# Performance work log

Hardware: AMD Instinct MI355X
Metric: run time of the kernel (lower is better)

Reference implementation:

```python
import jax, jax.numpy as jnp
import numpy as np

B, C, H, W = 8, 256, 128, 128
BN_EPS = 1e-5

def setup_inputs() -> dict:
    key = jax.random.key(0)
    ks = jax.random.split(key, 7)
    scale = 1.0 / np.sqrt(C)
    x = jax.random.normal(ks[0], (B, C, H, W), dtype=jnp.float32)
    w_qkv = jax.random.normal(ks[1], (3 * C, C), dtype=jnp.float32) * scale
    w_proj = jax.random.normal(ks[2], (C, C), dtype=jnp.float32) * scale
    gamma = jax.random.uniform(ks[3], (C,), dtype=jnp.float32)
    beta = jax.random.normal(ks[4], (C,), dtype=jnp.float32)
    running_mean = jax.random.normal(ks[5], (C,), dtype=jnp.float32)
    running_var = jax.random.uniform(ks[6], (C,), dtype=jnp.float32) + 0.5
    return {"x": x, "w_qkv": w_qkv, "w_proj": w_proj, "gamma": gamma,
            "beta": beta, "running_mean": running_mean, "running_var": running_var}

def reference(x, w_qkv, w_proj, gamma, beta, running_mean, running_var):
    b, c, h, w = x.shape
    n = h * w
    xf = x.reshape(b, c, n)                       # flatten spatial
    # 1x1 conv == channel matmul: [3c,c] x [b,c,n] -> [b,3c,n]
    qkv = jnp.einsum('oc,bcn->bon', w_qkv, xf)
    q, k, v = jnp.split(qkv, 3, axis=1)           # each [b,c,n]
    k = jax.nn.softmax(k, axis=-1)                # softmax over spatial
    context = jnp.einsum('bcn,bdn->bcd', k, v)    # k @ v^T, [b,c,c]
    out = jnp.einsum('bcd,bcn->bdn', context, q)  # context^T @ q, [b,c,n]
    out = jnp.einsum('oc,bcn->bon', w_proj, out)  # 1x1 proj
    # BatchNorm (inference form with running stats)
    inv = gamma / jnp.sqrt(running_var + BN_EPS)
    out = out * inv[None, :, None] + (beta - running_mean * inv)[None, :, None]
    out = jax.nn.relu(out)
    return out.reshape(b, c, h, w)
```

## Files before the change

### kernel.cpp

```cpp
#include <hip/hip_runtime.h>
#include <stdint.h>

#define B_   8
#define C_   256
#define N_   16384

typedef __attribute__((ext_vector_type(8))) short bf16x8;
typedef __attribute__((ext_vector_type(4))) float f32x4;

__device__ inline float bf2f(unsigned short h) {
    return __uint_as_float(((unsigned)h) << 16);
}
__device__ inline unsigned short f2bf(float f) {
    unsigned u = __float_as_uint(f);
    u += 0x7FFF + ((u >> 16) & 1);
    return (unsigned short)(u >> 16);
}

__device__ inline void gl_lds16(const void* g, void* l) {
    __builtin_amdgcn_global_load_lds(
        reinterpret_cast<const __attribute__((address_space(1))) unsigned int*>(
            reinterpret_cast<uintptr_t>(g)),
        reinterpret_cast<__attribute__((address_space(3))) unsigned int*>(
            reinterpret_cast<uintptr_t>(l)),
        16, 0, 0);
}

__device__ inline f32x4 mfma16(bf16x8 a, bf16x8 b, f32x4 c) {
    return __builtin_amdgcn_mfma_f32_16x16x32_bf16(a, b, c, 0, 0, 0);
}

__global__ __launch_bounds__(256) void k1_transpose(const float* __restrict__ x,
                                                    unsigned short* __restrict__ xT) {
    __shared__ unsigned short tile[64][65];
    const int b = blockIdx.z, c0 = blockIdx.y * 64, n0 = blockIdx.x * 64;
    const float* xb = x + (size_t)b * C_ * N_;
    const int t = threadIdx.x;
    const int tr = t >> 4, tc4 = (t & 15) * 4;
#pragma unroll
    for (int p = 0; p < 4; p++) {
        const int i = p * 16 + tr;
        const float4 v = *(const float4*)(xb + (size_t)(c0 + i) * N_ + n0 + tc4);
        tile[i][tc4 + 0] = f2bf(v.x);
        tile[i][tc4 + 1] = f2bf(v.y);
        tile[i][tc4 + 2] = f2bf(v.z);
        tile[i][tc4 + 3] = f2bf(v.w);
    }
    __syncthreads();
    unsigned short* xTb = xT + (size_t)b * N_ * C_;
#pragma unroll
    for (int p = 0; p < 4; p++) {
        const int jj = p * 16 + tr;
        ushort4 o;
        o.x = tile[tc4 + 0][jj];
        o.y = tile[tc4 + 1][jj];
        o.z = tile[tc4 + 2][jj];
        o.w = tile[tc4 + 3][jj];
        *(ushort4*)(xTb + (size_t)(n0 + jj) * C_ + c0 + tc4) = o;
    }
}

__global__ __launch_bounds__(256) void k1b_setup(const float* __restrict__ wqkv,
                                                 const float* __restrict__ gamma,
                                                 const float* __restrict__ beta,
                                                 const float* __restrict__ rmean,
                                                 const float* __restrict__ rvar,
                                                 unsigned short* __restrict__ wqkv_bf,
                                                 float* __restrict__ inv,
                                                 float* __restrict__ b2) {
    const int t = threadIdx.x;
    if (blockIdx.x < 192) {
        const int base = blockIdx.x * 1024 + t * 4;
        const float4 v = *(const float4*)(wqkv + base);
        ushort4 o;
        o.x = f2bf(v.x); o.y = f2bf(v.y); o.z = f2bf(v.z); o.w = f2bf(v.w);
        *(ushort4*)(wqkv_bf + base) = o;
    } else {
        const float iv = gamma[t] * rsqrtf(rvar[t] + 1e-5f);
        inv[t] = iv;
        b2[t]  = beta[t] - rmean[t] * iv;
    }
}

__global__ __launch_bounds__(256) void k2_kv(const unsigned short* __restrict__ Wkv,
                                             const unsigned short* __restrict__ xT,
                                             unsigned short* __restrict__ kL,
                                             unsigned short* __restrict__ v) {
    __shared__ __align__(16) unsigned short As[128 * 32];
    __shared__ __align__(16) unsigned short Bs[128 * 32];
    const int b  = blockIdx.z;
    const int m0 = blockIdx.y * 128;
    const int n0 = blockIdx.x * 128;
    const int t = threadIdx.x, wave = t >> 6, lane = t & 63;
    const int wm = wave >> 1, wn = wave & 1;

    const unsigned short* xTb = xT + (size_t)b * N_ * C_;

    const int ch1 = wave * 64 + lane, ch2 = ch1 + 256;
    const int r1 = ch1 >> 2, q1 = ch1 & 3;
    const int r2 = ch2 >> 2, q2 = ch2 & 3;
    unsigned short* ldsA1 = As + wave * 512;
    unsigned short* ldsA2 = As + 2048 + wave * 512;
    unsigned short* ldsB1 = Bs + wave * 512;
    unsigned short* ldsB2 = Bs + 2048 + wave * 512;

    f32x4 acc[4][4];
#pragma unroll
    for (int i = 0; i < 4; i++)
#pragma unroll
        for (int j = 0; j < 4; j++)
#pragma unroll
            for (int r = 0; r < 4; r++) acc[i][j][r] = 0.f;

    const int fr = lane & 15;
    const int fk = (lane >> 4) * 8;

    for (int kk = 0; kk < 256; kk += 32) {
        __syncthreads();
        gl_lds16(Wkv + (size_t)(m0 + r1) * 256 + kk + q1 * 8, ldsA1);
        gl_lds16(Wkv + (size_t)(m0 + r2) * 256 + kk + q2 * 8, ldsA2);
        gl_lds16(xTb + (size_t)(n0 + r1) * 256 + kk + q1 * 8, ldsB1);
        gl_lds16(xTb + (size_t)(n0 + r2) * 256 + kk + q2 * 8, ldsB2);
        __syncthreads();
        bf16x8 af[4], bfv[4];
#pragma unroll
        for (int i = 0; i < 4; i++)
            af[i] = *(const bf16x8*)(As + (wm * 64 + i * 16 + fr) * 32 + fk);
#pragma unroll
        for (int j = 0; j < 4; j++)
            bfv[j] = *(const bf16x8*)(Bs + (wn * 64 + j * 16 + fr) * 32 + fk);
#pragma unroll
        for (int i = 0; i < 4; i++)
#pragma unroll
            for (int j = 0; j < 4; j++)
                acc[i][j] = mfma16(af[i], bfv[j], acc[i][j]);
    }

    const int col = lane & 15, rowq = (lane >> 4) * 4;
    unsigned short* outK = kL + (size_t)b * C_ * N_;
    unsigned short* outV = v  + (size_t)b * C_ * N_;
#pragma unroll
    for (int i = 0; i < 4; i++) {
        const int gm = m0 + wm * 64 + i * 16 + rowq;
#pragma unroll
        for (int j = 0; j < 4; j++) {
            const int gn = n0 + wn * 64 + j * 16 + col;
#pragma unroll
            for (int r = 0; r < 4; r++) {
                const int m = gm + r;
                const unsigned short hv = f2bf(acc[i][j][r]);
                if (m < 256) outK[(size_t)m * N_ + gn] = hv;
                else         outV[(size_t)(m - 256) * N_ + gn] = hv;
            }
        }
    }
}

__global__ __launch_bounds__(256) void k3_stats(const unsigned short* __restrict__ kL,
                                                float* __restrict__ rmax,
                                                float* __restrict__ rsum) {
    const size_t rowbase = (size_t)blockIdx.x * N_;
    const int t = threadIdx.x;
    uint4 d[8];
#pragma unroll
    for (int i = 0; i < 8; i++)
        d[i] = *(const uint4*)(kL + rowbase + (size_t)(i * 256 + t) * 8);
    float m = -3.4e38f;
#pragma unroll
    for (int i = 0; i < 8; i++) {
        const unsigned short* p = (const unsigned short*)&d[i];
#pragma unroll
        for (int e = 0; e < 8; e++) m = fmaxf(m, bf2f(p[e]));
    }
#pragma unroll
    for (int o = 1; o < 64; o <<= 1) m = fmaxf(m, __shfl_xor(m, o, 64));
    __shared__ float red[4];
    __shared__ float red2[4];
    if ((t & 63) == 0) red[t >> 6] = m;
    __syncthreads();
    m = fmaxf(fmaxf(red[0], red[1]), fmaxf(red[2], red[3]));
    float s = 0.f;
#pragma unroll
    for (int i = 0; i < 8; i++) {
        const unsigned short* p = (const unsigned short*)&d[i];
#pragma unroll
        for (int e = 0; e < 8; e++) s += __expf(bf2f(p[e]) - m);
    }
#pragma unroll
    for (int o = 1; o < 64; o <<= 1) s += __shfl_xor(s, o, 64);
    if ((t & 63) == 0) red2[t >> 6] = s;
    __syncthreads();
    if (t == 0) {
        rmax[blockIdx.x] = m;
        rsum[blockIdx.x] = red2[0] + red2[1] + red2[2] + red2[3];
    }
}

__global__ __launch_bounds__(256) void k4_ctx(const unsigned short* __restrict__ kL,
                                              const unsigned short* __restrict__ v,
                                              const float* __restrict__ rmax,
                                              float* __restrict__ ctx) {
    __shared__ __align__(16) unsigned short As[128 * 32];
    __shared__ __align__(16) unsigned short Bs[128 * 32];
    const int bz = blockIdx.z;
    const int b = bz >> 3, s = bz & 7;
    const int m0 = blockIdx.y * 128;
    const int n0 = blockIdx.x * 128;
    const int t = threadIdx.x, wave = t >> 6, lane = t & 63;
    const int wm = wave >> 1, wn = wave & 1;

    const unsigned short* kb = kL + (size_t)b * C_ * N_;
    const unsigned short* vb = v  + (size_t)b * C_ * N_;

    const int ch1 = wave * 64 + lane, ch2 = ch1 + 256;
    const int r1 = ch1 >> 2, q1 = ch1 & 3;
    const int r2 = ch2 >> 2, q2 = ch2 & 3;
    const float mx1 = rmax[b * 256 + m0 + r1];
    const float mx2 = rmax[b * 256 + m0 + r2];
    unsigned short* ldsB1 = Bs + wave * 512;
    unsigned short* ldsB2 = Bs + 2048 + wave * 512;

    f32x4 acc[4][4];
#pragma unroll
    for (int i = 0; i < 4; i++)
#pragma unroll
        for (int j = 0; j < 4; j++)
#pragma unroll
            for (int r = 0; r < 4; r++) acc[i][j][r] = 0.f;

    const int fr = lane & 15;
    const int fk = (lane >> 4) * 8;
    const int kbase = s * 2048;

    for (int kk = kbase; kk < kbase + 2048; kk += 32) {
        __syncthreads();
        gl_lds16(vb + (size_t)(n0 + r1) * N_ + kk + q1 * 8, ldsB1);
        gl_lds16(vb + (size_t)(n0 + r2) * N_ + kk + q2 * 8, ldsB2);
        const uint4 a1 = *(const uint4*)(kb + (size_t)(m0 + r1) * N_ + kk + q1 * 8);
        const uint4 a2 = *(const uint4*)(kb + (size_t)(m0 + r2) * N_ + kk + q2 * 8);
        uint4 e1, e2;
        {
            const unsigned short* p = (const unsigned short*)&a1;
            unsigned short* o = (unsigned short*)&e1;
#pragma unroll
            for (int e = 0; e < 8; e++) o[e] = f2bf(__expf(bf2f(p[e]) - mx1));
        }
        {
            const unsigned short* p = (const unsigned short*)&a2;
            unsigned short* o = (unsigned short*)&e2;
#pragma unroll
            for (int e = 0; e < 8; e++) o[e] = f2bf(__expf(bf2f(p[e]) - mx2));
        }
        *(uint4*)(As + r1 * 32 + q1 * 8) = e1;
        *(uint4*)(As + r2 * 32 + q2 * 8) = e2;
        __syncthreads();
        bf16x8 af[4], bfv[4];
#pragma unroll
        for (int i = 0; i < 4; i++)
            af[i] = *(const bf16x8*)(As + (wm * 64 + i * 16 + fr) * 32 + fk);
#pragma unroll
        for (int j = 0; j < 4; j++)
            bfv[j] = *(const bf16x8*)(Bs + (wn * 64 + j * 16 + fr) * 32 + fk);
#pragma unroll
        for (int i = 0; i < 4; i++)
#pragma unroll
            for (int j = 0; j < 4; j++)
                acc[i][j] = mfma16(af[i], bfv[j], acc[i][j]);
    }

    float* cb = ctx + (size_t)b * C_ * C_;
    const int col = lane & 15, rowq = (lane >> 4) * 4;
#pragma unroll
    for (int i = 0; i < 4; i++) {
        const int gc = m0 + wm * 64 + i * 16 + rowq;
#pragma unroll
        for (int j = 0; j < 4; j++) {
            const int gd = n0 + wn * 64 + j * 16 + col;
#pragma unroll
            for (int r = 0; r < 4; r++)
                atomicAdd(&cb[(size_t)(gc + r) * C_ + gd], acc[i][j][r]);
        }
    }
}

__global__ __launch_bounds__(256) void k5a_T(const float* __restrict__ Wp,
                                             const float* __restrict__ ctx,
                                             const float* __restrict__ rsum,
                                             float* __restrict__ T) {
    __shared__ float Asm[64][65];
    __shared__ float Bsm[64][65];
    const int b = blockIdx.z;
    const int o0 = blockIdx.y * 64, c0 = blockIdx.x * 64;
    const int t = threadIdx.x;
    const int tm = t >> 4, tn = t & 15;
    const int lc4 = tn * 4;
    float acc[4][4] = {};
    const float* cb = ctx + (size_t)b * C_ * C_;
    for (int kk = 0; kk < 256; kk += 64) {
        __syncthreads();
#pragma unroll
        for (int p = 0; p < 4; p++) {
            const int r = p * 16 + tm;
            const float4 av = *(const float4*)(Wp + (size_t)(o0 + r) * C_ + kk + lc4);
            Asm[r][lc4] = av.x; Asm[r][lc4 + 1] = av.y; Asm[r][lc4 + 2] = av.z; Asm[r][lc4 + 3] = av.w;
            const float4 bv = *(const float4*)(cb + (size_t)(c0 + r) * C_ + kk + lc4);
            Bsm[r][lc4] = bv.x; Bsm[r][lc4 + 1] = bv.y; Bsm[r][lc4 + 2] = bv.z; Bsm[r][lc4 + 3] = bv.w;
        }
        __syncthreads();
        for (int k = 0; k < 64; k++) {
            float a_[4], b_[4];
#pragma unroll
            for (int i = 0; i < 4; i++) a_[i] = Asm[tm * 4 + i][k];
#pragma unroll
            for (int j = 0; j < 4; j++) b_[j] = Bsm[tn * 4 + j][k];
#pragma unroll
            for (int i = 0; i < 4; i++)
#pragma unroll
                for (int j = 0; j < 4; j++) acc[i][j] += a_[i] * b_[j];
        }
    }
    float isv[4];
#pragma unroll
    for (int j = 0; j < 4; j++) isv[j] = 1.f / rsum[b * 256 + c0 + tn * 4 + j];
#pragma unroll
    for (int i = 0; i < 4; i++)
#pragma unroll
        for (int j = 0; j < 4; j++)
            T[((size_t)b * C_ + o0 + tm * 4 + i) * C_ + c0 + tn * 4 + j] = acc[i][j] * isv[j];
}

__global__ __launch_bounds__(256) void k5b_G(const float* __restrict__ Tm,
                                             const float* __restrict__ Wq,
                                             const float* __restrict__ inv,
                                             unsigned short* __restrict__ G) {
    __shared__ float Asm[64][65];
    __shared__ float Bsm[64][65];
    const int b = blockIdx.z;
    const int o0 = blockIdx.y * 64, j0 = blockIdx.x * 64;
    const int t = threadIdx.x;
    const int tm = t >> 4, tn = t & 15;
    const int lc4 = tn * 4;
    float acc[4][4] = {};
    const float* Tb = Tm + (size_t)b * C_ * C_;
    for (int kk = 0; kk < 256; kk += 64) {
        __syncthreads();
#pragma unroll
        for (int p = 0; p < 4; p++) {
            const int r = p * 16 + tm;
            const float4 av = *(const float4*)(Tb + (size_t)(o0 + r) * C_ + kk + lc4);
            Asm[r][lc4] = av.x; Asm[r][lc4 + 1] = av.y; Asm[r][lc4 + 2] = av.z; Asm[r][lc4 + 3] = av.w;
            const float4 bv = *(const float4*)(Wq + (size_t)(kk + r) * C_ + j0 + lc4);
            Bsm[r][lc4] = bv.x; Bsm[r][lc4 + 1] = bv.y; Bsm[r][lc4 + 2] = bv.z; Bsm[r][lc4 + 3] = bv.w;
        }
        __syncthreads();
        for (int k = 0; k < 64; k++) {
            float a_[4], b_[4];
#pragma unroll
            for (int i = 0; i < 4; i++) a_[i] = Asm[tm * 4 + i][k];
#pragma unroll
            for (int j = 0; j < 4; j++) b_[j] = Bsm[k][tn * 4 + j];
#pragma unroll
            for (int i = 0; i < 4; i++)
#pragma unroll
                for (int j = 0; j < 4; j++) acc[i][j] += a_[i] * b_[j];
        }
    }
#pragma unroll
    for (int i = 0; i < 4; i++) {
        const float iv = inv[o0 + tm * 4 + i];
#pragma unroll
        for (int j = 0; j < 4; j++)
            G[((size_t)b * C_ + o0 + tm * 4 + i) * C_ + j0 + tn * 4 + j] = f2bf(acc[i][j] * iv);
    }
}

__global__ __launch_bounds__(256) void k6_out(const unsigned short* __restrict__ G,
                                              const unsigned short* __restrict__ xT,
                                              const float* __restrict__ b2,
                                              float* __restrict__ out) {
    __shared__ __align__(16) unsigned short As[128 * 32];
    __shared__ __align__(16) unsigned short Bs[128 * 32];
    const int b  = blockIdx.z;
    const int m0 = blockIdx.y * 128;
    const int n0 = blockIdx.x * 128;
    const int t = threadIdx.x, wave = t >> 6, lane = t & 63;
    const int wm = wave >> 1, wn = wave & 1;

    const unsigned short* Gb  = G  + (size_t)b * C_ * C_;
    const unsigned short* xTb = xT + (size_t)b * N_ * C_;

    const int ch1 = wave * 64 + lane, ch2 = ch1 + 256;
    const int r1 = ch1 >> 2, q1 = ch1 & 3;
    const int r2 = ch2 >> 2, q2 = ch2 & 3;
    unsigned short* ldsA1 = As + wave * 512;
    unsigned short* ldsA2 = As + 2048 + wave * 512;
    unsigned short* ldsB1 = Bs + wave * 512;
    unsigned short* ldsB2 = Bs + 2048 + wave * 512;

    f32x4 acc[4][4];
#pragma unroll
    for (int i = 0; i < 4; i++)
#pragma unroll
        for (int j = 0; j < 4; j++)
#pragma unroll
            for (int r = 0; r < 4; r++) acc[i][j][r] = 0.f;

    const int fr = lane & 15;
    const int fk = (lane >> 4) * 8;

    for (int kk = 0; kk < 256; kk += 32) {
        __syncthreads();
        gl_lds16(Gb  + (size_t)(m0 + r1) * 256 + kk + q1 * 8, ldsA1);
        gl_lds16(Gb  + (size_t)(m0 + r2) * 256 + kk + q2 * 8, ldsA2);
        gl_lds16(xTb + (size_t)(n0 + r1) * 256 + kk + q1 * 8, ldsB1);
        gl_lds16(xTb + (size_t)(n0 + r2) * 256 + kk + q2 * 8, ldsB2);
        __syncthreads();
        bf16x8 af[4], bfv[4];
#pragma unroll
        for (int i = 0; i < 4; i++)
            af[i] = *(const bf16x8*)(As + (wm * 64 + i * 16 + fr) * 32 + fk);
#pragma unroll
        for (int j = 0; j < 4; j++)
            bfv[j] = *(const bf16x8*)(Bs + (wn * 64 + j * 16 + fr) * 32 + fk);
#pragma unroll
        for (int i = 0; i < 4; i++)
#pragma unroll
            for (int j = 0; j < 4; j++)
                acc[i][j] = mfma16(af[i], bfv[j], acc[i][j]);
    }

    const int col = lane & 15, rowq = (lane >> 4) * 4;
    float* ob = out + (size_t)b * C_ * N_;
#pragma unroll
    for (int i = 0; i < 4; i++) {
        const int gm = m0 + wm * 64 + i * 16 + rowq;
#pragma unroll
        for (int j = 0; j < 4; j++) {
            const int gn = n0 + wn * 64 + j * 16 + col;
#pragma unroll
            for (int r = 0; r < 4; r++) {
                const float val = fmaxf(acc[i][j][r] + b2[gm + r], 0.f);
                ob[(size_t)(gm + r) * N_ + gn] = val;
            }
        }
    }
}

extern "C" void kernel_launch(void* const* d_in, const int* in_sizes, int n_in,
                              void* d_out, int out_size, void* d_ws, size_t ws_size,
                              hipStream_t stream) {
    const float* x     = (const float*)d_in[0];
    const float* wqkv  = (const float*)d_in[1];
    const float* wproj = (const float*)d_in[2];
    const float* gamma = (const float*)d_in[3];
    const float* beta  = (const float*)d_in[4];
    const float* rmean = (const float*)d_in[5];
    const float* rvar  = (const float*)d_in[6];
    float* out = (float*)d_out;

    char* ws = (char*)d_ws;
    size_t off = 0;
    auto alloc = [&](size_t bytes) {
        void* p = ws + off;
        off += (bytes + 255) & ~(size_t)255;
        return p;
    };
    unsigned short* xT      = (unsigned short*)alloc((size_t)B_ * N_ * C_ * 2);
    unsigned short* kL      = (unsigned short*)alloc((size_t)B_ * C_ * N_ * 2);
    unsigned short* vv      = (unsigned short*)alloc((size_t)B_ * C_ * N_ * 2);
    unsigned short* wqkv_bf = (unsigned short*)alloc((size_t)768 * 256 * 2);
    float* rmax = (float*)alloc(2048 * 4);
    float* rsum = (float*)alloc(2048 * 4);
    float* invp = (float*)alloc(256 * 4);
    float* b2p  = (float*)alloc(256 * 4);
    float* ctx  = (float*)alloc((size_t)B_ * C_ * C_ * 4);
    float* Tm   = (float*)alloc((size_t)B_ * C_ * C_ * 4);
    unsigned short* G = (unsigned short*)alloc((size_t)B_ * C_ * C_ * 2);

    hipLaunchKernelGGL(k1_transpose, dim3(256, 4, 8), dim3(256), 0, stream, x, xT);
    hipLaunchKernelGGL(k1b_setup, dim3(193), dim3(256), 0, stream,
                       wqkv, gamma, beta, rmean, rvar, wqkv_bf, invp, b2p);
    hipLaunchKernelGGL(k2_kv, dim3(128, 4, 8), dim3(256), 0, stream,
                       wqkv_bf + 256 * 256, xT, kL, vv);
    hipLaunchKernelGGL(k3_stats, dim3(2048), dim3(256), 0, stream, kL, rmax, rsum);
    hipMemsetAsync(ctx, 0, (size_t)B_ * C_ * C_ * 4, stream);
    hipLaunchKernelGGL(k4_ctx, dim3(2, 2, 64), dim3(256), 0, stream, kL, vv, rmax, ctx);
    hipLaunchKernelGGL(k5a_T, dim3(4, 4, 8), dim3(256), 0, stream, wproj, ctx, rsum, Tm);
    hipLaunchKernelGGL(k5b_G, dim3(4, 4, 8), dim3(256), 0, stream, Tm, wqkv, invp, G);
    hipLaunchKernelGGL(k6_out, dim3(128, 2, 8), dim3(256), 0, stream, G, xT, b2p, out);
}
```

Measured before the change: 447.7 us.

## Fuse softmax stats into KV GEMM and context kernels, stage full xT tile

Removes the separate k3_stats pass. The row max is now computed in the k2 epilogue through an order-preserving uint atomicMax, and the exp-sum is accumulated inside k4_ctx with atomicAdd. k2 and k6 now load a whole 128x256 bf16 xT tile into LDS once and loop over all output-channel chunks, reading the weight operands straight from global memory. This removes one full read of K and the repeated xT loads, at the cost of 64KB of LDS per block (lower occupancy), uncached global weight fragment loads, and atomics on the row statistics.

```diff
diff --git a/kernel.cpp b/kernel.cpp
--- a/kernel.cpp
+++ b/kernel.cpp
@@ -15,6 +15,14 @@
     unsigned u = __float_as_uint(f);
     u += 0x7FFF + ((u >> 16) & 1);
     return (unsigned short)(u >> 16);
+}
+__device__ inline unsigned fkey(float f) {
+    unsigned u = __float_as_uint(f);
+    return (u & 0x80000000u) ? ~u : (u | 0x80000000u);
+}
+__device__ inline float funkey(unsigned k) {
+    unsigned u = (k & 0x80000000u) ? (k ^ 0x80000000u) : ~k;
+    return __uint_as_float(u);
 }
 
 __device__ inline void gl_lds16(const void* g, void* l) {
@@ -85,121 +93,96 @@
 __global__ __launch_bounds__(256) void k2_kv(const unsigned short* __restrict__ Wkv,
                                              const unsigned short* __restrict__ xT,
                                              unsigned short* __restrict__ kL,
-                                             unsigned short* __restrict__ v) {
-    __shared__ __align__(16) unsigned short As[128 * 32];
-    __shared__ __align__(16) unsigned short Bs[128 * 32];
-    const int b  = blockIdx.z;
-    const int m0 = blockIdx.y * 128;
+                                             unsigned short* __restrict__ vv,
+                                             unsigned int* __restrict__ rmaxU) {
+    __shared__ __align__(16) unsigned short Bs[128 * 256];
+    const int b  = blockIdx.y;
     const int n0 = blockIdx.x * 128;
     const int t = threadIdx.x, wave = t >> 6, lane = t & 63;
     const int wm = wave >> 1, wn = wave & 1;
 
-    const unsigned short* xTb = xT + (size_t)b * N_ * C_;
-
-    const int ch1 = wave * 64 + lane, ch2 = ch1 + 256;
-    const int r1 = ch1 >> 2, q1 = ch1 & 3;
-    const int r2 = ch2 >> 2, q2 = ch2 & 3;
-    unsigned short* ldsA1 = As + wave * 512;
-    unsigned short* ldsA2 = As + 2048 + wave * 512;
-    unsigned short* ldsB1 = Bs + wave * 512;
-    unsigned short* ldsB2 = Bs + 2048 + wave * 512;
-
-    f32x4 acc[4][4];
-#pragma unroll
-    for (int i = 0; i < 4; i++)
-#pragma unroll
-        for (int j = 0; j < 4; j++)
-#pragma unroll
-            for (int r = 0; r < 4; r++) acc[i][j][r] = 0.f;
+    const unsigned short* xTb = xT + (size_t)b * N_ * C_ + (size_t)n0 * C_;
+#pragma unroll
+    for (int rnd = 0; rnd < 16; rnd++) {
+        gl_lds16(xTb + rnd * 2048 + wave * 512 + lane * 8,
+                 Bs + rnd * 2048 + wave * 512);
+    }
+    __syncthreads();
 
     const int fr = lane & 15;
     const int fk = (lane >> 4) * 8;
-
-    for (int kk = 0; kk < 256; kk += 32) {
-        __syncthreads();
-        gl_lds16(Wkv + (size_t)(m0 + r1) * 256 + kk + q1 * 8, ldsA1);
-        gl_lds16(Wkv + (size_t)(m0 + r2) * 256 + kk + q2 * 8, ldsA2);
-        gl_lds16(xTb + (size_t)(n0 + r1) * 256 + kk + q1 * 8, ldsB1);
-        gl_lds16(xTb + (size_t)(n0 + r2) * 256 + kk + q2 * 8, ldsB2);
-        __syncthreads();
-        bf16x8 af[4], bfv[4];
-#pragma unroll
-        for (int i = 0; i < 4; i++)
-            af[i] = *(const bf16x8*)(As + (wm * 64 + i * 16 + fr) * 32 + fk);
-#pragma unroll
-        for (int j = 0; j < 4; j++)
-            bfv[j] = *(const bf16x8*)(Bs + (wn * 64 + j * 16 + fr) * 32 + fk);
-#pragma unroll
-        for (int i = 0; i < 4; i++)
-#pragma unroll
-            for (int j = 0; j < 4; j++)
-                acc[i][j] = mfma16(af[i], bfv[j], acc[i][j]);
-    }
-
     const int col = lane & 15, rowq = (lane >> 4) * 4;
     unsigned short* outK = kL + (size_t)b * C_ * N_;
-    unsigned short* outV = v  + (size_t)b * C_ * N_;
-#pragma unroll
-    for (int i = 0; i < 4; i++) {
-        const int gm = m0 + wm * 64 + i * 16 + rowq;
-#pragma unroll
-        for (int j = 0; j < 4; j++) {
-            const int gn = n0 + wn * 64 + j * 16 + col;
-#pragma unroll
-            for (int r = 0; r < 4; r++) {
-                const int m = gm + r;
-                const unsigned short hv = f2bf(acc[i][j][r]);
-                if (m < 256) outK[(size_t)m * N_ + gn] = hv;
-                else         outV[(size_t)(m - 256) * N_ + gn] = hv;
+    unsigned short* outV = vv + (size_t)b * C_ * N_;
+
+    for (int mc = 0; mc < 4; mc++) {
+        const int mbase = mc * 128;
+        f32x4 acc[4][4];
+#pragma unroll
+        for (int i = 0; i < 4; i++)
+#pragma unroll
+            for (int j = 0; j < 4; j++)
+#pragma unroll
+                for (int r = 0; r < 4; r++) acc[i][j][r] = 0.f;
+
+#pragma unroll
+        for (int kk = 0; kk < 256; kk += 32) {
+            bf16x8 af[4], bfv[4];
+#pragma unroll
+            for (int i = 0; i < 4; i++)
+                af[i] = *(const bf16x8*)(Wkv + (size_t)(mbase + wm * 64 + i * 16 + fr) * 256 + kk + fk);
+#pragma unroll
+            for (int j = 0; j < 4; j++)
+                bfv[j] = *(const bf16x8*)(Bs + (wn * 64 + j * 16 + fr) * 256 + kk + fk);
+#pragma unroll
+            for (int i = 0; i < 4; i++)
+#pragma unroll
+                for (int j = 0; j < 4; j++)
+                    acc[i][j] = mfma16(af[i], bfv[j], acc[i][j]);
+        }
+
+        if (mc < 2) {
+#pragma unroll
+            for (int i = 0; i < 4; i++) {
+                const int gm = mbase + wm * 64 + i * 16 + rowq;
+#pragma unroll
+                for (int r = 0; r < 4; r++) {
+                    float vmax = -3.4e38f;
+#pragma unroll
+                    for (int j = 0; j < 4; j++) {
+                        const int gn = n0 + wn * 64 + j * 16 + col;
+                        const unsigned short hv = f2bf(acc[i][j][r]);
+                        outK[(size_t)(gm + r) * N_ + gn] = hv;
+                        vmax = fmaxf(vmax, bf2f(hv));
+                    }
+#pragma unroll
+                    for (int o = 1; o < 16; o <<= 1)
+                        vmax = fmaxf(vmax, __shfl_xor(vmax, o, 64));
+                    if (col == 0)
+                        atomicMax(&rmaxU[b * 256 + gm + r], fkey(vmax));
+                }
             }
-        }
-    }
-}
-
-__global__ __launch_bounds__(256) void k3_stats(const unsigned short* __restrict__ kL,
-                                                float* __restrict__ rmax,
-                                                float* __restrict__ rsum) {
-    const size_t rowbase = (size_t)blockIdx.x * N_;
-    const int t = threadIdx.x;
-    uint4 d[8];
-#pragma unroll
-    for (int i = 0; i < 8; i++)
-        d[i] = *(const uint4*)(kL + rowbase + (size_t)(i * 256 + t) * 8);
-    float m = -3.4e38f;
-#pragma unroll
-    for (int i = 0; i < 8; i++) {
-        const unsigned short* p = (const unsigned short*)&d[i];
-#pragma unroll
-        for (int e = 0; e < 8; e++) m = fmaxf(m, bf2f(p[e]));
-    }
-#pragma unroll
-    for (int o = 1; o < 64; o <<= 1) m = fmaxf(m, __shfl_xor(m, o, 64));
-    __shared__ float red[4];
-    __shared__ float red2[4];
-    if ((t & 63) == 0) red[t >> 6] = m;
-    __syncthreads();
-    m = fmaxf(fmaxf(red[0], red[1]), fmaxf(red[2], red[3]));
-    float s = 0.f;
-#pragma unroll
-    for (int i = 0; i < 8; i++) {
-        const unsigned short* p = (const unsigned short*)&d[i];
-#pragma unroll
-        for (int e = 0; e < 8; e++) s += __expf(bf2f(p[e]) - m);
-    }
-#pragma unroll
-    for (int o = 1; o < 64; o <<= 1) s += __shfl_xor(s, o, 64);
-    if ((t & 63) == 0) red2[t >> 6] = s;
-    __syncthreads();
-    if (t == 0) {
-        rmax[blockIdx.x] = m;
-        rsum[blockIdx.x] = red2[0] + red2[1] + red2[2] + red2[3];
+        } else {
+#pragma unroll
+            for (int i = 0; i < 4; i++) {
+                const int gm = mbase - 256 + wm * 64 + i * 16 + rowq;
+#pragma unroll
+                for (int j = 0; j < 4; j++) {
+                    const int gn = n0 + wn * 64 + j * 16 + col;
+#pragma unroll
+                    for (int r = 0; r < 4; r++)
+                        outV[(size_t)(gm + r) * N_ + gn] = f2bf(acc[i][j][r]);
+                }
+            }
+        }
     }
 }
 
 __global__ __launch_bounds__(256) void k4_ctx(const unsigned short* __restrict__ kL,
                                               const unsigned short* __restrict__ v,
-                                              const float* __restrict__ rmax,
-                                              float* __restrict__ ctx) {
+                                              const unsigned int* __restrict__ rmaxU,
+                                              float* __restrict__ ctx,
+                                              float* __restrict__ rsum) {
     __shared__ __align__(16) unsigned short As[128 * 32];
     __shared__ __align__(16) unsigned short Bs[128 * 32];
     const int bz = blockIdx.z;
@@ -215,8 +198,8 @@
     const int ch1 = wave * 64 + lane, ch2 = ch1 + 256;
     const int r1 = ch1 >> 2, q1 = ch1 & 3;
     const int r2 = ch2 >> 2, q2 = ch2 & 3;
-    const float mx1 = rmax[b * 256 + m0 + r1];
-    const float mx2 = rmax[b * 256 + m0 + r2];
+    const float mx1 = funkey(rmaxU[b * 256 + m0 + r1]);
+    const float mx2 = funkey(rmaxU[b * 256 + m0 + r2]);
     unsigned short* ldsB1 = Bs + wave * 512;
     unsigned short* ldsB2 = Bs + 2048 + wave * 512;
 
@@ -228,6 +211,7 @@
 #pragma unroll
             for (int r = 0; r < 4; r++) acc[i][j][r] = 0.f;
 
+    float sacc1 = 0.f, sacc2 = 0.f;
     const int fr = lane & 15;
     const int fk = (lane >> 4) * 8;
     const int kbase = s * 2048;
@@ -243,13 +227,21 @@
             const unsigned short* p = (const unsigned short*)&a1;
             unsigned short* o = (unsigned short*)&e1;
 #pragma unroll
-            for (int e = 0; e < 8; e++) o[e] = f2bf(__expf(bf2f(p[e]) - mx1));
+            for (int e = 0; e < 8; e++) {
+                const float ev = __expf(bf2f(p[e]) - mx1);
+                sacc1 += ev;
+                o[e] = f2bf(ev);
+            }
         }
         {
             const unsigned short* p = (const unsigned short*)&a2;
             unsigned short* o = (unsigned short*)&e2;
 #pragma unroll
-            for (int e = 0; e < 8; e++) o[e] = f2bf(__expf(bf2f(p[e]) - mx2));
+            for (int e = 0; e < 8; e++) {
+                const float ev = __expf(bf2f(p[e]) - mx2);
+                sacc2 += ev;
+                o[e] = f2bf(ev);
+            }
         }
         *(uint4*)(As + r1 * 32 + q1 * 8) = e1;
         *(uint4*)(As + r2 * 32 + q2 * 8) = e2;
@@ -266,6 +258,17 @@
 #pragma unroll
             for (int j = 0; j < 4; j++)
                 acc[i][j] = mfma16(af[i], bfv[j], acc[i][j]);
+    }
+
+    if (blockIdx.x == 0) {
+        sacc1 += __shfl_xor(sacc1, 1, 64);
+        sacc1 += __shfl_xor(sacc1, 2, 64);
+        sacc2 += __shfl_xor(sacc2, 1, 64);
+        sacc2 += __shfl_xor(sacc2, 2, 64);
+        if ((lane & 3) == 0) {
+            atomicAdd(&rsum[b * 256 + m0 + r1], sacc1);
+            atomicAdd(&rsum[b * 256 + m0 + r2], sacc2);
+        }
     }
 
     float* cb = ctx + (size_t)b * C_ * C_;
@@ -378,69 +381,63 @@
                                               const unsigned short* __restrict__ xT,
                                               const float* __restrict__ b2,
                                               float* __restrict__ out) {
-    __shared__ __align__(16) unsigned short As[128 * 32];
-    __shared__ __align__(16) unsigned short Bs[128 * 32];
-    const int b  = blockIdx.z;
-    const int m0 = blockIdx.y * 128;
+    __shared__ __align__(16) unsigned short Bs[128 * 256];
+    const int b  = blockIdx.y;
     const int n0 = blockIdx.x * 128;
     const int t = threadIdx.x, wave = t >> 6, lane = t & 63;
     const int wm = wave >> 1, wn = wave & 1;
 
-    const unsigned short* Gb  = G  + (size_t)b * C_ * C_;
-    const unsigned short* xTb = xT + (size_t)b * N_ * C_;
-
-    const int ch1 = wave * 64 + lane, ch2 = ch1 + 256;
-    const int r1 = ch1 >> 2, q1 = ch1 & 3;
-    const int r2 = ch2 >> 2, q2 = ch2 & 3;
-    unsigned short* ldsA1 = As + wave * 512;
-    unsigned short* ldsA2 = As + 2048 + wave * 512;
-    unsigned short* ldsB1 = Bs + wave * 512;
-    unsigned short* ldsB2 = Bs + 2048 + wave * 512;
-
-    f32x4 acc[4][4];
-#pragma unroll
-    for (int i = 0; i < 4; i++)
-#pragma unroll
-        for (int j = 0; j < 4; j++)
-#pragma unroll
-            for (int r = 0; r < 4; r++) acc[i][j][r] = 0.f;
+    const unsigned short* Gb  = G + (size_t)b * C_ * C_;
+    const unsigned short* xTb = xT + (size_t)b * N_ * C_ + (size_t)n0 * C_;
+#pragma unroll
+    for (int rnd = 0; rnd < 16; rnd++) {
+        gl_lds16(xTb + rnd * 2048 + wave * 512 + lane * 8,
+                 Bs + rnd * 2048 + wave * 512);
+    }
+    __syncthreads();
 
     const int fr = lane & 15;
     const int fk = (lane >> 4) * 8;
-
-    for (int kk = 0; kk < 256; kk += 32) {
-        __syncthreads();
-        gl_lds16(Gb  + (size_t)(m0 + r1) * 256 + kk + q1 * 8, ldsA1);
-        gl_lds16(Gb  + (size_t)(m0 + r2) * 256 + kk + q2 * 8, ldsA2);
-        gl_lds16(xTb + (size_t)(n0 + r1) * 256 + kk + q1 * 8, ldsB1);
-        gl_lds16(xTb + (size_t)(n0 + r2) * 256 + kk + q2 * 8, ldsB2);
-        __syncthreads();
-        bf16x8 af[4], bfv[4];
-#pragma unroll
-        for (int i = 0; i < 4; i++)
-            af[i] = *(const bf16x8*)(As + (wm * 64 + i * 16 + fr) * 32 + fk);
-#pragma unroll
-        for (int j = 0; j < 4; j++)
-            bfv[j] = *(const bf16x8*)(Bs + (wn * 64 + j * 16 + fr) * 32 + fk);
-#pragma unroll
-        for (int i = 0; i < 4; i++)
-#pragma unroll
-            for (int j = 0; j < 4; j++)
-                acc[i][j] = mfma16(af[i], bfv[j], acc[i][j]);
-    }
-
     const int col = lane & 15, rowq = (lane >> 4) * 4;
     float* ob = out + (size_t)b * C_ * N_;
-#pragma unroll
-    for (int i = 0; i < 4; i++) {
-        const int gm = m0 + wm * 64 + i * 16 + rowq;
-#pragma unroll
-        for (int j = 0; j < 4; j++) {
-            const int gn = n0 + wn * 64 + j * 16 + col;
-#pragma unroll
-            for (int r = 0; r < 4; r++) {
-                const float val = fmaxf(acc[i][j][r] + b2[gm + r], 0.f);
-                ob[(size_t)(gm + r) * N_ + gn] = val;
+
+    for (int mc = 0; mc < 2; mc++) {
+        const int mbase = mc * 128;
+        f32x4 acc[4][4];
+#pragma unroll
+        for (int i = 0; i < 4; i++)
+#pragma unroll
+            for (int j = 0; j < 4; j++)
+#pragma unroll
+                for (int r = 0; r < 4; r++) acc[i][j][r] = 0.f;
+
+#pragma unroll
+        for (int kk = 0; kk < 256; kk += 32) {
+            bf16x8 af[4], bfv[4];
+#pragma unroll
+            for (int i = 0; i < 4; i++)
+                af[i] = *(const bf16x8*)(Gb + (size_t)(mbase + wm * 64 + i * 16 + fr) * 256 + kk + fk);
+#pragma unroll
+            for (int j = 0; j < 4; j++)
+                bfv[j] = *(const bf16x8*)(Bs + (wn * 64 + j * 16 + fr) * 256 + kk + fk);
+#pragma unroll
+            for (int i = 0; i < 4; i++)
+#pragma unroll
+                for (int j = 0; j < 4; j++)
+                    acc[i][j] = mfma16(af[i], bfv[j], acc[i][j]);
+        }
+
+#pragma unroll
+        for (int i = 0; i < 4; i++) {
+            const int gm = mbase + wm * 64 + i * 16 + rowq;
+#pragma unroll
+            for (int j = 0; j < 4; j++) {
+                const int gn = n0 + wn * 64 + j * 16 + col;
+#pragma unroll
+                for (int r = 0; r < 4; r++) {
+                    const float val = fmaxf(acc[i][j][r] + b2[gm + r], 0.f);
+                    ob[(size_t)(gm + r) * N_ + gn] = val;
+                }
             }
         }
     }
@@ -465,27 +462,29 @@
         off += (bytes + 255) & ~(size_t)255;
         return p;
     };
+    float*        ctx   = (float*)alloc((size_t)B_ * C_ * C_ * 4);
+    unsigned int* rmaxU = (unsigned int*)alloc(2048 * 4);
+    float*        rsum  = (float*)alloc(2048 * 4);
+    const size_t  zero_bytes = (size_t)B_ * C_ * C_ * 4 + 2 * 2048 * 4 + 512;
+
     unsigned short* xT      = (unsigned short*)alloc((size_t)B_ * N_ * C_ * 2);
     unsigned short* kL      = (unsigned short*)alloc((size_t)B_ * C_ * N_ * 2);
-    unsigned short* vv      = (unsigned short*)alloc((size_t)B_ * C_ * N_ * 2);
+    unsigned short* vvp     = (unsigned short*)alloc((size_t)B_ * C_ * N_ * 2);
     unsigned short* wqkv_bf = (unsigned short*)alloc((size_t)768 * 256 * 2);
-    float* rmax = (float*)alloc(2048 * 4);
-    float* rsum = (float*)alloc(2048 * 4);
     float* invp = (float*)alloc(256 * 4);
     float* b2p  = (float*)alloc(256 * 4);
-    float* ctx  = (float*)alloc((size_t)B_ * C_ * C_ * 4);
     float* Tm   = (float*)alloc((size_t)B_ * C_ * C_ * 4);
     unsigned short* G = (unsigned short*)alloc((size_t)B_ * C_ * C_ * 2);
 
+    hipMemsetAsync(ctx, 0, zero_bytes, stream);
     hipLaunchKernelGGL(k1_transpose, dim3(256, 4, 8), dim3(256), 0, stream, x, xT);
     hipLaunchKernelGGL(k1b_setup, dim3(193), dim3(256), 0, stream,
                        wqkv, gamma, beta, rmean, rvar, wqkv_bf, invp, b2p);
-    hipLaunchKernelGGL(k2_kv, dim3(128, 4, 8), dim3(256), 0, stream,
-                       wqkv_bf + 256 * 256, xT, kL, vv);
-    hipLaunchKernelGGL(k3_stats, dim3(2048), dim3(256), 0, stream, kL, rmax, rsum);
-    hipMemsetAsync(ctx, 0, (size_t)B_ * C_ * C_ * 4, stream);
-    hipLaunchKernelGGL(k4_ctx, dim3(2, 2, 64), dim3(256), 0, stream, kL, vv, rmax, ctx);
+    hipLaunchKernelGGL(k2_kv, dim3(128, 8), dim3(256), 0, stream,
+                       wqkv_bf + 256 * 256, xT, kL, vvp, rmaxU);
+    hipLaunchKernelGGL(k4_ctx, dim3(2, 2, 64), dim3(256), 0, stream,
+                       kL, vvp, rmaxU, ctx, rsum);
     hipLaunchKernelGGL(k5a_T, dim3(4, 4, 8), dim3(256), 0, stream, wproj, ctx, rsum, Tm);
     hipLaunchKernelGGL(k5b_G, dim3(4, 4, 8), dim3(256), 0, stream, Tm, wqkv, invp, G);
-    hipLaunchKernelGGL(k6_out, dim3(128, 2, 8), dim3(256), 0, stream, G, xT, b2p, out);
-}
+    hipLaunchKernelGGL(k6_out, dim3(128, 8), dim3(256), 0, stream, G, xT, b2p, out);
+}
```

New measurement: 535.9 us. +19.7%, slower.
